# Kernel tuning notes

Hardware: AMD Instinct MI355X
Metric: run time of the kernel (lower is better)

Reference implementation:

```python
import jax, jax.numpy as jnp
import numpy as np

BN_EPS = 1e-5
L1_EPS = 1e-12


def setup_inputs() -> dict:
    key = jax.random.key(0)
    ks = jax.random.split(key, 3)
    T, N, F = 8, 256, 128
    node_feats = jax.random.normal(ks[0], (T, N, F), dtype=jnp.float32)
    # 1x1 conv weights, no bias: [out=F, in=2F]
    w1 = jax.random.normal(ks[1], (F, 2 * F), dtype=jnp.float32) * (1.0 / np.sqrt(2 * F))
    w2 = jax.random.normal(ks[2], (F, 2 * F), dtype=jnp.float32) * (1.0 / np.sqrt(2 * F))
    g1 = jnp.ones((F,), jnp.float32)
    b1 = jnp.zeros((F,), jnp.float32)
    g2 = jnp.ones((F,), jnp.float32)
    b2 = jnp.zeros((F,), jnp.float32)
    return {"node_feats": node_feats, "w1": w1, "g1": g1, "b1": b1,
            "w2": w2, "g2": g2, "b2": b2}


def _branch(x_ij, w, g, b):
    # 1x1 conv == per-pair matmul: [T,N,N,2F] @ [F,2F]^T -> [T,N,N,F]
    y = jnp.einsum('tnmc,fc->tnmf', x_ij, w)
    # BatchNorm2d (train mode): stats over batch and both spatial dims, biased var
    mean = jnp.mean(y, axis=(0, 1, 2))
    var = jnp.var(y, axis=(0, 1, 2))
    y = (y - mean) * jax.lax.rsqrt(var + BN_EPS) * g + b
    return jax.nn.relu(y)


def reference(node_feats, w1, g1, b1, w2, g2, b2):
    T, N, F = node_feats.shape
    # pairwise broadcast-concat: x_ij[t,i,j] = [x[t,i], x[t,j]]
    x_i = jnp.broadcast_to(node_feats[:, :, None, :], (T, N, N, F))
    x_j = jnp.broadcast_to(node_feats[:, None, :, :], (T, N, N, F))
    x_ij = jnp.concatenate([x_i, x_j], axis=-1)  # [T,N,N,2F]

    sim = _branch(x_ij, w1, g1, b1)[:, None]   # [T,1,N,N,F]
    dsim = _branch(x_ij, w2, g2, b2)[:, None]  # [T,1,N,N,F]
    edge = jnp.concatenate([sim, dsim], axis=1)  # [T,2,N,N,F]

    # zero the diagonal (i == j)
    diag_mask = (1.0 - jnp.eye(N, dtype=node_feats.dtype))[None, None, :, :, None]
    edge = edge * diag_mask

    # L1 normalize along last dim (F.normalize p=1)
    l1 = jnp.sum(jnp.abs(edge), axis=-1, keepdims=True)
    return edge / jnp.maximum(l1, L1_EPS)
```

## Files before the change

kernel.cpp:

```cpp
#include <hip/hip_runtime.h>


#define TT 8
#define NN 256
#define FF 128

typedef float vf4 __attribute__((ext_vector_type(4)));

__global__ __launch_bounds__(128) void k_matmul(
    const float* __restrict__ x,
    const float* __restrict__ w1,
    const float* __restrict__ w2,
    float* __restrict__ ws)
{
    __shared__ float xs[4][FF];
    const int tid = threadIdx.x;
    const int row0 = blockIdx.x * 4;

    {
        const float4* xv = (const float4*)(x + row0 * FF);
        float4 q = xv[tid];
        ((float4*)&xs[0][0])[tid] = q;
    }
    __syncthreads();

    const int f = tid;
    float acc0[4] = {0,0,0,0}, acc1[4] = {0,0,0,0};
    float acc2[4] = {0,0,0,0}, acc3[4] = {0,0,0,0};
    const float4* w1v = (const float4*)w1;
    const float4* w2v = (const float4*)w2;

    #pragma unroll 8
    for (int c4 = 0; c4 < 32; ++c4) {
        float4 qa1 = w1v[f * 64 + c4];
        float4 qb1 = w1v[f * 64 + 32 + c4];
        float4 qa2 = w2v[f * 64 + c4];
        float4 qb2 = w2v[f * 64 + 32 + c4];
        const int c = c4 * 4;
        #pragma unroll
        for (int r = 0; r < 4; ++r) {
            float x0 = xs[r][c], x1 = xs[r][c + 1], x2 = xs[r][c + 2], x3 = xs[r][c + 3];
            acc0[r] = fmaf(x0, qa1.x, fmaf(x1, qa1.y, fmaf(x2, qa1.z, fmaf(x3, qa1.w, acc0[r]))));
            acc1[r] = fmaf(x0, qb1.x, fmaf(x1, qb1.y, fmaf(x2, qb1.z, fmaf(x3, qb1.w, acc1[r]))));
            acc2[r] = fmaf(x0, qa2.x, fmaf(x1, qa2.y, fmaf(x2, qa2.z, fmaf(x3, qa2.w, acc2[r]))));
            acc3[r] = fmaf(x0, qb2.x, fmaf(x1, qb2.y, fmaf(x2, qb2.z, fmaf(x3, qb2.w, acc3[r]))));
        }
    }

    float* A1 = ws;
    float* B1 = ws + 262144;
    float* A2 = ws + 524288;
    float* B2 = ws + 786432;
    #pragma unroll
    for (int r = 0; r < 4; ++r) {
        int row = row0 + r;
        A1[row * FF + f] = acc0[r];
        B1[row * FF + f] = acc1[r];
        A2[row * FF + f] = acc2[r];
        B2[row * FF + f] = acc3[r];
    }
}

__global__ __launch_bounds__(256) void k_stats(
    const float* __restrict__ ab,
    float* __restrict__ sums, float* __restrict__ sumsq)
{
    const int bx = blockIdx.x;
    const int t = bx & 7, arr = bx >> 3;
    const float* A = ab + arr * 262144 + t * NN * FF;
    const int tid = threadIdx.x;
    const int f = tid & 127, h = tid >> 7;
    float s = 0.f, q = 0.f;
    for (int n = h; n < NN; n += 2) {
        float v = A[n * FF + f];
        s += v;
        q = fmaf(v, v, q);
    }
    __shared__ float ls[256], lq[256];
    ls[tid] = s; lq[tid] = q;
    __syncthreads();
    if (tid < 128) {
        sums [(arr * 8 + t) * FF + f] = ls[tid] + ls[tid + 128];
        sumsq[(arr * 8 + t) * FF + f] = lq[tid] + lq[tid + 128];
    }
}

__global__ __launch_bounds__(256) void k_scale(
    const float* __restrict__ sums, const float* __restrict__ sumsq,
    const float* __restrict__ g1, const float* __restrict__ b1,
    const float* __restrict__ g2, const float* __restrict__ b2,
    float* __restrict__ scale, float* __restrict__ bias)
{
    const int tid = threadIdx.x;
    const int br = tid >> 7, f = tid & 127;
    const int aA = 2 * br, aB = 2 * br + 1;
    float SA = 0.f, SB = 0.f, QA = 0.f, QB = 0.f, cross = 0.f;
    #pragma unroll
    for (int t = 0; t < TT; ++t) {
        float sa = sums[(aA * 8 + t) * FF + f];
        float sb = sums[(aB * 8 + t) * FF + f];
        SA += sa; SB += sb;
        cross = fmaf(sa, sb, cross);
        QA += sumsq[(aA * 8 + t) * FF + f];
        QB += sumsq[(aB * 8 + t) * FF + f];
    }
    const float invTN  = 1.0f / 2048.0f;
    const float invTNN = 1.0f / 262144.0f;
    float mA = SA * invTN, mB = SB * invTN;
    float m = mA + mB;
    float ey2 = (QA + QB) * invTN + cross * invTNN;
    float var = ey2 - m * m;
    float gf = br ? g2[f] : g1[f];
    float bf = br ? b2[f] : b1[f];
    float sc = gf * rsqrtf(var + 1e-5f);
    scale[br * FF + f] = sc;
    bias [br * FF + f] = bf - m * sc;
}

__global__ __launch_bounds__(256) void k_edge(
    const float* __restrict__ ws,
    const float* __restrict__ scale, const float* __restrict__ bias,
    float* __restrict__ out)
{
    const int bx = blockIdx.x;
    const int i  = bx & 255;
    const int br = (bx >> 8) & 1;
    const int t  = bx >> 9;
    const int tid = threadIdx.x;

    const float* A = ws + (2 * br) * 262144 + (t * NN + i) * FF;
    const float* B = ws + (2 * br + 1) * 262144 + t * NN * FF;

    __shared__ vf4 sc_lds[FF / 4];
    __shared__ vf4 cc_lds[FF / 4];
    __shared__ float r_lds[NN];

    if (tid < FF) {
        float sf = scale[br * FF + tid];
        float cf = fmaf(A[tid], sf, bias[br * FF + tid]);
        ((float*)sc_lds)[tid] = sf;
        ((float*)cc_lds)[tid] = cf;
    }
    __syncthreads();

    {
        const vf4* Bj = (const vf4*)(B + tid * FF);
        float sum = 0.f;
        #pragma unroll 8
        for (int f4 = 0; f4 < FF / 4; ++f4) {
            vf4 b = Bj[f4];
            vf4 s = sc_lds[f4];
            vf4 c = cc_lds[f4];
            sum += fmaxf(fmaf(b.x, s.x, c.x), 0.f)
                 + fmaxf(fmaf(b.y, s.y, c.y), 0.f)
                 + fmaxf(fmaf(b.z, s.z, c.z), 0.f)
                 + fmaxf(fmaf(b.w, s.w, c.w), 0.f);
        }
        r_lds[tid] = 1.0f / fmaxf(sum, 1e-12f);
    }
    __syncthreads();

    const int wave = tid >> 6, lane = tid & 63;
    const int fo = (lane & 31) * 4;
    const int jh = lane >> 5;

    const vf4 s4 = *(const vf4*)((const float*)sc_lds + fo);
    const vf4 c4 = *(const vf4*)((const float*)cc_lds + fo);

    vf4* obase = (vf4*)(out + ((size_t)(t * 2 + br) * NN + i) * (size_t)NN * FF);

    #pragma unroll 4
    for (int jj = 0; jj < 32; ++jj) {
        const int j = wave * 64 + jj * 2 + jh;
        vf4 b = *(const vf4*)(B + j * FF + fo);
        float r = r_lds[j];
        r = (j == i) ? 0.0f : r;
        vf4 v;
        v.x = fmaxf(fmaf(b.x, s4.x, c4.x), 0.f) * r;
        v.y = fmaxf(fmaf(b.y, s4.y, c4.y), 0.f) * r;
        v.z = fmaxf(fmaf(b.z, s4.z, c4.z), 0.f) * r;
        v.w = fmaxf(fmaf(b.w, s4.w, c4.w), 0.f) * r;
        __builtin_nontemporal_store(v, &obase[(size_t)j * 32 + (lane & 31)]);
    }
}

extern "C" void kernel_launch(void* const* d_in, const int* in_sizes, int n_in,
                              void* d_out, int out_size, void* d_ws, size_t ws_size,
                              hipStream_t stream)
{
    const float* x  = (const float*)d_in[0];
    const float* w1 = (const float*)d_in[1];
    const float* g1 = (const float*)d_in[2];
    const float* b1 = (const float*)d_in[3];
    const float* w2 = (const float*)d_in[4];
    const float* g2 = (const float*)d_in[5];
    const float* b2 = (const float*)d_in[6];

    float* ws    = (float*)d_ws;
    float* sums  = ws + 1048576;
    float* sumsq = sums + 4096;
    float* scale = sumsq + 4096;
    float* bias  = scale + 256;
    float* out = (float*)d_out;

    k_matmul<<<512, 128, 0, stream>>>(x, w1, w2, ws);
    k_stats <<<32, 256, 0, stream>>>(ws, sums, sumsq);
    k_scale <<<1, 256, 0, stream>>>(sums, sumsq, g1, b1, g2, b2, scale, bias);
    k_edge  <<<4096, 256, 0, stream>>>(ws, scale, bias, out);
}
```

Measured before the change: 600.4 us.

## Store transposed B projections and coalesce per-row L1 sum in edge kernel

The matmul kernel now computes 8 rows per block and also writes the B projections in a transposed [T][F][N] layout. The edge kernel's L1-norm pass reads that transposed copy with coalesced vector loads across j, splitting the feature range over four waves and reducing the partials through shared memory. Previously each thread read its own 512-byte row, a strided access pattern. The trade-off is extra workspace, extra transposed writes, and halved matmul grid occupancy. The output write phase, which dominates the 268MB output, is unchanged.

Measured after the change: 572.6 us. -4.6%, faster.

```diff
diff --git a/kernel.cpp b/kernel.cpp
--- a/kernel.cpp
+++ b/kernel.cpp
@@ -13,24 +13,26 @@
     const float* __restrict__ w2,
     float* __restrict__ ws)
 {
-    __shared__ float xs[4][FF];
-    const int tid = threadIdx.x;
-    const int row0 = blockIdx.x * 4;
+    __shared__ float xs[8][FF];
+    const int tid = threadIdx.x;
+    const int row0 = blockIdx.x * 8;
 
     {
         const float4* xv = (const float4*)(x + row0 * FF);
-        float4 q = xv[tid];
-        ((float4*)&xs[0][0])[tid] = q;
+        ((float4*)xs)[tid]       = xv[tid];
+        ((float4*)xs)[tid + 128] = xv[tid + 128];
     }
     __syncthreads();
 
     const int f = tid;
-    float acc0[4] = {0,0,0,0}, acc1[4] = {0,0,0,0};
-    float acc2[4] = {0,0,0,0}, acc3[4] = {0,0,0,0};
+    float acc0[8], acc1[8], acc2[8], acc3[8];
+    #pragma unroll
+    for (int r = 0; r < 8; ++r) { acc0[r]=0.f; acc1[r]=0.f; acc2[r]=0.f; acc3[r]=0.f; }
+
     const float4* w1v = (const float4*)w1;
     const float4* w2v = (const float4*)w2;
 
-    #pragma unroll 8
+    #pragma unroll 4
     for (int c4 = 0; c4 < 32; ++c4) {
         float4 qa1 = w1v[f * 64 + c4];
         float4 qb1 = w1v[f * 64 + 32 + c4];
@@ -38,7 +40,7 @@
         float4 qb2 = w2v[f * 64 + 32 + c4];
         const int c = c4 * 4;
         #pragma unroll
-        for (int r = 0; r < 4; ++r) {
+        for (int r = 0; r < 8; ++r) {
             float x0 = xs[r][c], x1 = xs[r][c + 1], x2 = xs[r][c + 2], x3 = xs[r][c + 3];
             acc0[r] = fmaf(x0, qa1.x, fmaf(x1, qa1.y, fmaf(x2, qa1.z, fmaf(x3, qa1.w, acc0[r]))));
             acc1[r] = fmaf(x0, qb1.x, fmaf(x1, qb1.y, fmaf(x2, qb1.z, fmaf(x3, qb1.w, acc1[r]))));
@@ -52,12 +54,27 @@
     float* A2 = ws + 524288;
     float* B2 = ws + 786432;
     #pragma unroll
-    for (int r = 0; r < 4; ++r) {
+    for (int r = 0; r < 8; ++r) {
         int row = row0 + r;
         A1[row * FF + f] = acc0[r];
         B1[row * FF + f] = acc1[r];
         A2[row * FF + f] = acc2[r];
         B2[row * FF + f] = acc3[r];
+    }
+
+    {
+        const int t  = row0 >> 8;
+        const int n0 = row0 & 255;
+        float* b1t = ws + 1048576 + (t * FF + f) * NN + n0;
+        float* b2t = ws + 1310720 + (t * FF + f) * NN + n0;
+        vf4 p0 = {acc1[0], acc1[1], acc1[2], acc1[3]};
+        vf4 p1 = {acc1[4], acc1[5], acc1[6], acc1[7]};
+        vf4 q0 = {acc3[0], acc3[1], acc3[2], acc3[3]};
+        vf4 q1 = {acc3[4], acc3[5], acc3[6], acc3[7]};
+        *(vf4*)(b1t)     = p0;
+        *(vf4*)(b1t + 4) = p1;
+        *(vf4*)(b2t)     = q0;
+        *(vf4*)(b2t + 4) = q1;
     }
 }
 
@@ -128,35 +145,50 @@
     const int t  = bx >> 9;
     const int tid = threadIdx.x;
 
-    const float* A = ws + (2 * br) * 262144 + (t * NN + i) * FF;
-    const float* B = ws + (2 * br + 1) * 262144 + t * NN * FF;
-
-    __shared__ vf4 sc_lds[FF / 4];
-    __shared__ vf4 cc_lds[FF / 4];
+    const float* A  = ws + (2 * br) * 262144 + (t * NN + i) * FF;
+    const float* B  = ws + (2 * br + 1) * 262144 + t * NN * FF;
+    const float* Bt = ws + 1048576 + br * 262144 + t * FF * NN;
+
+    __shared__ float sc_lds[FF];
+    __shared__ float cc_lds[FF];
+    __shared__ vf4   part[4][NN / 4];
     __shared__ float r_lds[NN];
 
     if (tid < FF) {
         float sf = scale[br * FF + tid];
         float cf = fmaf(A[tid], sf, bias[br * FF + tid]);
-        ((float*)sc_lds)[tid] = sf;
-        ((float*)cc_lds)[tid] = cf;
-    }
-    __syncthreads();
-
-    {
-        const vf4* Bj = (const vf4*)(B + tid * FF);
-        float sum = 0.f;
+        sc_lds[tid] = sf;
+        cc_lds[tid] = cf;
+    }
+    __syncthreads();
+
+    {
+        const int jq = tid & 63;
+        const int fq = tid >> 6;
+        const float* bt = Bt + (fq * 32) * NN + jq * 4;
+        float s0 = 0.f, s1 = 0.f, s2 = 0.f, s3 = 0.f;
         #pragma unroll 8
-        for (int f4 = 0; f4 < FF / 4; ++f4) {
-            vf4 b = Bj[f4];
-            vf4 s = sc_lds[f4];
-            vf4 c = cc_lds[f4];
-            sum += fmaxf(fmaf(b.x, s.x, c.x), 0.f)
-                 + fmaxf(fmaf(b.y, s.y, c.y), 0.f)
-                 + fmaxf(fmaf(b.z, s.z, c.z), 0.f)
-                 + fmaxf(fmaf(b.w, s.w, c.w), 0.f);
+        for (int ff = 0; ff < 32; ++ff) {
+            vf4 b = *(const vf4*)(bt + ff * NN);
+            const int f = fq * 32 + ff;
+            float sf = sc_lds[f];
+            float cf = cc_lds[f];
+            s0 += fmaxf(fmaf(b.x, sf, cf), 0.f);
+            s1 += fmaxf(fmaf(b.y, sf, cf), 0.f);
+            s2 += fmaxf(fmaf(b.z, sf, cf), 0.f);
+            s3 += fmaxf(fmaf(b.w, sf, cf), 0.f);
         }
-        r_lds[tid] = 1.0f / fmaxf(sum, 1e-12f);
+        vf4 p = {s0, s1, s2, s3};
+        part[fq][jq] = p;
+    }
+    __syncthreads();
+    {
+        const float* p0 = (const float*)&part[0][0];
+        const float* p1 = (const float*)&part[1][0];
+        const float* p2 = (const float*)&part[2][0];
+        const float* p3 = (const float*)&part[3][0];
+        float l1 = p0[tid] + p1[tid] + p2[tid] + p3[tid];
+        r_lds[tid] = 1.0f / fmaxf(l1, 1e-12f);
     }
     __syncthreads();
 
@@ -164,8 +196,8 @@
     const int fo = (lane & 31) * 4;
     const int jh = lane >> 5;
 
-    const vf4 s4 = *(const vf4*)((const float*)sc_lds + fo);
-    const vf4 c4 = *(const vf4*)((const float*)cc_lds + fo);
+    const vf4 s4 = *(const vf4*)(sc_lds + fo);
+    const vf4 c4 = *(const vf4*)(cc_lds + fo);
 
     vf4* obase = (vf4*)(out + ((size_t)(t * 2 + br) * NN + i) * (size_t)NN * FF);
 
@@ -197,13 +229,13 @@
     const float* b2 = (const float*)d_in[6];
 
     float* ws    = (float*)d_ws;
-    float* sums  = ws + 1048576;
+    float* sums  = ws + 1572864;
     float* sumsq = sums + 4096;
     float* scale = sumsq + 4096;
     float* bias  = scale + 256;
     float* out = (float*)d_out;
 
-    k_matmul<<<512, 128, 0, stream>>>(x, w1, w2, ws);
+    k_matmul<<<256, 128, 0, stream>>>(x, w1, w2, ws);
     k_stats <<<32, 256, 0, stream>>>(ws, sums, sumsq);
     k_scale <<<1, 256, 0, stream>>>(sums, sumsq, g1, b1, g2, b2, scale, bias);
     k_edge  <<<4096, 256, 0, stream>>>(ws, scale, bias, out);
```
